# Kernel optimization log

Measured on AMD Instinct MI355X. Metric: run time of the kernel, lower is better.

Reference implementation:

```python
import jax, jax.numpy as jnp
import numpy as np

B, T, C, H = 2, 2048, 1024, 16
HD = C // H  # head_dim = 64


def setup_inputs() -> dict:
    key = jax.random.key(0)
    ks = jax.random.split(key, 5)
    x = jax.random.normal(ks[0], (B, T, C), dtype=jnp.float32)
    # realistic rotary tables: cos/sin of position*inv_freq, shape (T, HD//2)
    inv_freq = 1.0 / (10000.0 ** (jnp.arange(0, HD, 2, dtype=jnp.float32) / HD))
    ang = jnp.arange(T, dtype=jnp.float32)[:, None] * inv_freq[None, :]
    cos, sin = jnp.cos(ang), jnp.sin(ang)
    w_attn = jax.random.normal(ks[1], (C, 3 * C), dtype=jnp.float32) * (C ** -0.5)
    b_attn = jnp.zeros((3 * C,), dtype=jnp.float32)
    w_proj = jax.random.normal(ks[2], (C, C), dtype=jnp.float32) * (C ** -0.5)
    b_proj = jnp.zeros((C,), dtype=jnp.float32)
    return {"x": x, "cos": cos, "sin": sin, "w_attn": w_attn, "b_attn": b_attn,
            "w_proj": w_proj, "b_proj": b_proj}


def _apply_rotary(x, cos, sin):
    # x: (B, H, T, HD); cos/sin: (T, HD//2) broadcast over B,H
    x_even = x[..., ::2]
    x_odd = x[..., 1::2]
    rot = jnp.stack((x_even * cos - x_odd * sin, x_even * sin + x_odd * cos), axis=-1)
    return rot.reshape(*x.shape[:-1], x.shape[-1])


def reference(x, cos, sin, w_attn, b_attn, w_proj, b_proj):
    b, t, c = x.shape
    qkv = x @ w_attn + b_attn                       # (B, T, 3C)
    q, k, v = jnp.split(qkv, 3, axis=-1)
    # (B, T, C) -> (B, H, T, HD)
    def to_heads(z):
        return z.reshape(b, t, H, HD).transpose(0, 2, 1, 3)
    q, k, v = to_heads(q), to_heads(k), to_heads(v)
    q = _apply_rotary(q, cos, sin)
    k = _apply_rotary(k, cos, sin)
    scale = 1.0 / jnp.sqrt(jnp.asarray(HD, dtype=x.dtype))
    scores = jnp.einsum('bhqd,bhkd->bhqk', q, k) * scale
    causal = jnp.tril(jnp.ones((t, t), dtype=bool))
    scores = jnp.where(causal, scores, jnp.asarray(-jnp.inf, dtype=scores.dtype))
    attn = jax.nn.softmax(scores, axis=-1)
    y = jnp.einsum('bhqk,bhkd->bhqd', attn, v)      # (B, H, T, HD)
    y = y.transpose(0, 2, 1, 3).reshape(b, t, c)
    return y @ w_proj + b_proj
```

## Files before the change

kernel.cpp:

```cpp
#include <hip/hip_runtime.h>
#include <hip/hip_bf16.h>
#include <math.h>

#define Bsz 2
#define Tseq 2048
#define Cdim 1024
#define Hn 16
#define HDim 64
#define Mrows 4096
#define N3 3072
#define QSCALE 0.1803368801111137f

typedef __bf16 bf16_t;
typedef __bf16 bf16x4 __attribute__((ext_vector_type(4)));
typedef __bf16 bf16x8 __attribute__((ext_vector_type(8)));
typedef float floatx4 __attribute__((ext_vector_type(4)));

__device__ __forceinline__ void async16(const void* g, void* l) {
    __builtin_amdgcn_global_load_lds(
        (const __attribute__((address_space(1))) void*)g,
        (__attribute__((address_space(3))) void*)l, 16, 0, 0);
}

__global__ __launch_bounds__(256) void prep_kernel(
    const float* __restrict__ x, const float* __restrict__ w_attn,
    const float* __restrict__ w_proj, bf16_t* __restrict__ xb,
    bf16_t* __restrict__ waT, bf16_t* __restrict__ wpT)
{
    __shared__ float Ts[32][33];
    const int bid = blockIdx.x;
    if (bid < 2048) {
        size_t g = (size_t)bid * 256 + threadIdx.x;
        float4 a = *(const float4*)(x + g * 8);
        float4 b = *(const float4*)(x + g * 8 + 4);
        bf16x8 o;
        o[0] = (bf16_t)a.x; o[1] = (bf16_t)a.y; o[2] = (bf16_t)a.z; o[3] = (bf16_t)a.w;
        o[4] = (bf16_t)b.x; o[5] = (bf16_t)b.y; o[6] = (bf16_t)b.z; o[7] = (bf16_t)b.w;
        *(bf16x8*)(xb + g * 8) = o;
        return;
    }
    const float* in; bf16_t* out; int R, C, bx, by;
    if (bid < 5120) {
        int t = bid - 2048; in = w_attn; out = waT; R = Cdim; C = N3;
        bx = t % 96; by = t / 96;
    } else {
        int t = bid - 5120; in = w_proj; out = wpT; R = Cdim; C = Cdim;
        bx = t & 31; by = t >> 5;
    }
    int c0 = bx << 5, r0 = by << 5;
    int lr = threadIdx.x >> 3, lc = (threadIdx.x & 7) << 2;
    float4 v = *(const float4*)(in + (size_t)(r0 + lr) * C + c0 + lc);
    Ts[lr][lc] = v.x; Ts[lr][lc + 1] = v.y; Ts[lr][lc + 2] = v.z; Ts[lr][lc + 3] = v.w;
    __syncthreads();
    bf16x4 o;
    o[0] = (bf16_t)Ts[lc + 0][lr]; o[1] = (bf16_t)Ts[lc + 1][lr];
    o[2] = (bf16_t)Ts[lc + 2][lr]; o[3] = (bf16_t)Ts[lc + 3][lr];
    *(bf16x4*)(out + (size_t)(c0 + lr) * R + r0 + lc) = o;
}

__global__ __launch_bounds__(256) void gemm_qkv(
    const bf16_t* __restrict__ xb, const bf16_t* __restrict__ waT,
    const float* __restrict__ bias, const float* __restrict__ cosb,
    const float* __restrict__ sinb,
    bf16_t* __restrict__ qb, bf16_t* __restrict__ kb, bf16_t* __restrict__ vt)
{
    __shared__ bf16_t As[128 * 32];
    __shared__ bf16_t Bs[128 * 32];
    const int tid = threadIdx.x;
    const int lane = tid & 63, w = tid >> 6;
    const int lm = lane & 15, quad = lane >> 4;
    const int wy = w >> 1, wx = w & 1;
    const int m0 = blockIdx.y << 7, n0 = blockIdx.x << 7;

    const floatx4 fz = {0.f, 0.f, 0.f, 0.f};
    floatx4 acc[4][4];
    #pragma unroll
    for (int i = 0; i < 4; i++)
        #pragma unroll
        for (int j = 0; j < 4; j++) acc[i][j] = fz;

    const bf16_t* Ag = xb + (size_t)m0 * Cdim;
    const bf16_t* Bg = waT + (size_t)n0 * Cdim;

    for (int k0 = 0; k0 < Cdim; k0 += 32) {
        #pragma unroll
        for (int it = 0; it < 2; ++it) {
            int ci = (w << 7) + (it << 6) + lane;
            int row = ci >> 2, cq = (ci & 3) ^ (row & 3);
            async16(Ag + (size_t)row * Cdim + k0 + cq * 8, As + ((w << 7) + (it << 6)) * 8);
            async16(Bg + (size_t)row * Cdim + k0 + cq * 8, Bs + ((w << 7) + (it << 6)) * 8);
        }
        __syncthreads();
        bf16x8 af[4], bfr[4];
        #pragma unroll
        for (int i = 0; i < 4; i++) {
            int row = (wy << 6) + (i << 4) + lm;
            int cq = quad ^ (lm & 3);
            af[i] = *(const bf16x8*)&As[row * 32 + cq * 8];
        }
        #pragma unroll
        for (int j = 0; j < 4; j++) {
            int row = (wx << 6) + (j << 4) + lm;
            int cq = quad ^ (lm & 3);
            bfr[j] = *(const bf16x8*)&Bs[row * 32 + cq * 8];
        }
        #pragma unroll
        for (int i = 0; i < 4; i++)
            #pragma unroll
            for (int j = 0; j < 4; j++)
                acc[i][j] = __builtin_amdgcn_mfma_f32_16x16x32_bf16(af[i], bfr[j], acc[i][j], 0, 0, 0);
        __syncthreads();
    }

    const int sec = n0 >> 10;
    const int mb = m0 + (wy << 6);
    const int nb = n0 + (wx << 6);
    #pragma unroll
    for (int i = 0; i < 4; i++) {
        int mrow0 = mb + (i << 4) + (quad << 2);
        int b = mrow0 >> 11, t0 = mrow0 & 2047;
        #pragma unroll
        for (int j = 0; j < 4; j++) {
            int n = nb + (j << 4) + lm;
            float bi = bias[n];
            int rel = n & 1023;
            int h = rel >> 6, hd = rel & 63;
            if (sec == 2) {
                int tp = (t0 & ~31) | (((t0 >> 2) & 3) << 3) | (((t0 >> 4) & 1) << 2);
                bf16x4 pk;
                #pragma unroll
                for (int r = 0; r < 4; r++) pk[r] = (bf16_t)(acc[i][j][r] + bi);
                *(bf16x4*)&vt[((size_t)(b * Hn + h) * HDim + hd) * Tseq + tp] = pk;
            } else {
                bf16_t* dst = (sec == 0) ? qb : kb;
                const int ih = hd >> 1;
                const bool ev = !(hd & 1);
                #pragma unroll
                for (int r = 0; r < 4; r++) {
                    int t = t0 + r;
                    float v = acc[i][j][r] + bi;
                    float x = __shfl_xor(v, 1);
                    float c = cosb[t * 32 + ih], s = sinb[t * 32 + ih];
                    float rv = ev ? (v * c - x * s) : (x * s + v * c);
                    if (sec == 0) rv *= QSCALE;
                    dst[((size_t)(b * Hn + h) * Tseq + t) * HDim + hd] = (bf16_t)rv;
                }
            }
        }
    }
}

__global__ __launch_bounds__(256) void attn_mfma(
    const bf16_t* __restrict__ qb, const bf16_t* __restrict__ kb,
    const bf16_t* __restrict__ vt, bf16_t* __restrict__ yb)
{
    __shared__ bf16_t Ks[2][64 * 64];
    __shared__ bf16_t VTs[2][64 * 64];

    const int pp = blockIdx.x & 15;
    const int bh = blockIdx.x >> 4;
    const int b = bh >> 4, h = bh & 15;
    const int tid = threadIdx.x;
    const int w4 = tid >> 6, lane = tid & 63, lm = lane & 15, quad = lane >> 4;
    const int jt0 = pp, jt1 = 31 - pp;
    const int nk = 32 - pp;

    {
        const bf16_t* Kg = kb + (size_t)bh * Tseq * HDim;
        const bf16_t* Vg = vt + (size_t)bh * HDim * Tseq;
        #pragma unroll
        for (int it = 0; it < 2; ++it) {
            int ci = (it << 8) + tid;
            int row = ci >> 3, cq = (ci & 7) ^ (row & 7);
            async16(Kg + row * HDim + cq * 8, &Ks[0][((it << 8) + (w4 << 6)) * 8]);
            async16(Vg + (size_t)row * Tseq + cq * 8, &VTs[0][((it << 8) + (w4 << 6)) * 8]);
        }
    }

    bf16x8 qf[2][2];
    #pragma unroll
    for (int t = 0; t < 2; ++t) {
        int qrow = ((t ? jt1 : jt0) << 6) + (w4 << 4) + lm;
        const bf16_t* Qg = qb + ((size_t)bh * Tseq + qrow) * HDim;
        #pragma unroll
        for (int ks = 0; ks < 2; ++ks)
            qf[t][ks] = *(const bf16x8*)(Qg + (ks << 5) + (quad << 3));
    }
    __syncthreads();

    const floatx4 fz = {0.f, 0.f, 0.f, 0.f};
    floatx4 o_[2][4];
    #pragma unroll
    for (int t = 0; t < 2; ++t)
        #pragma unroll
        for (int f = 0; f < 4; ++f) o_[t][f] = fz;
    float l_[2] = {0.f, 0.f};
    const int lastk[2] = {pp, 31 - pp};
    const int qq[2] = {(jt0 << 6) + (w4 << 4) + lm, (jt1 << 6) + (w4 << 4) + lm};

    for (int kt = 0; kt < nk; ++kt) {
        const int cb = kt & 1;
        if (kt + 1 < nk) {
            const int nb2 = cb ^ 1;
            const bf16_t* Kg = kb + ((size_t)bh * Tseq + ((kt + 1) << 6)) * HDim;
            const bf16_t* Vg = vt + (size_t)bh * HDim * Tseq + ((kt + 1) << 6);
            #pragma unroll
            for (int it = 0; it < 2; ++it) {
                int ci = (it << 8) + tid;
                int row = ci >> 3, cq = (ci & 7) ^ (row & 7);
                async16(Kg + row * HDim + cq * 8, &Ks[nb2][((it << 8) + (w4 << 6)) * 8]);
                async16(Vg + (size_t)row * Tseq + cq * 8, &VTs[nb2][((it << 8) + (w4 << 6)) * 8]);
            }
        }

        floatx4 st[2][4];
        #pragma unroll
        for (int t = 0; t < 2; ++t)
            #pragma unroll
            for (int sub = 0; sub < 4; ++sub) st[t][sub] = fz;
        #pragma unroll
        for (int ks = 0; ks < 2; ++ks) {
            bf16x8 kf[4];
            #pragma unroll
            for (int sub = 0; sub < 4; ++sub) {
                int krow = (sub << 4) + lm;
                int kc = ((ks << 2) + quad) ^ (krow & 7);
                kf[sub] = *(const bf16x8*)&Ks[cb][krow * 64 + kc * 8];
            }
            if (kt <= lastk[0])
                #pragma unroll
                for (int sub = 0; sub < 4; ++sub)
                    st[0][sub] = __builtin_amdgcn_mfma_f32_16x16x32_bf16(
                        kf[sub], qf[0][ks], st[0][sub], 0, 0, 0);
            #pragma unroll
            for (int sub = 0; sub < 4; ++sub)
                st[1][sub] = __builtin_amdgcn_mfma_f32_16x16x32_bf16(
                    kf[sub], qf[1][ks], st[1][sub], 0, 0, 0);
        }

        bf16x8 pf[2][2];
        #pragma unroll
        for (int t = 0; t < 2; ++t) {
            if (kt > lastk[t]) continue;
            const bool dm = (kt == lastk[t]);
            float rs = 0.f;
            #pragma unroll
            for (int cc = 0; cc < 2; ++cc)
                #pragma unroll
                for (int jj = 0; jj < 8; ++jj) {
                    int sub = (cc << 1) + (jj >> 2), r = jj & 3;
                    float val = st[t][sub][r];
                    if (dm) {
                        int key = (kt << 6) + (sub << 4) + (quad << 2) + r;
                        if (key > qq[t]) val = -3e38f;
                    }
                    float p = exp2f(val);
                    rs += p;
                    pf[t][cc][jj] = (bf16_t)p;
                }
            rs += __shfl_xor(rs, 16);
            rs += __shfl_xor(rs, 32);
            l_[t] += rs;
        }

        #pragma unroll
        for (int cc = 0; cc < 2; ++cc) {
            bf16x8 vf[4];
            #pragma unroll
            for (int f = 0; f < 4; ++f) {
                int vrow = (f << 4) + lm;
                int vc = ((cc << 2) + quad) ^ (vrow & 7);
                vf[f] = *(const bf16x8*)&VTs[cb][vrow * 64 + vc * 8];
            }
            #pragma unroll
            for (int t = 0; t < 2; ++t) {
                if (kt > lastk[t]) continue;
                #pragma unroll
                for (int f = 0; f < 4; ++f)
                    o_[t][f] = __builtin_amdgcn_mfma_f32_16x16x32_bf16(
                        vf[f], pf[t][cc], o_[t][f], 0, 0, 0);
            }
        }
        __syncthreads();
    }

    #pragma unroll
    for (int t = 0; t < 2; ++t) {
        float inv = 1.f / l_[t];
        size_t base = ((size_t)(b * Tseq) + qq[t]) * Cdim + (h << 6) + (quad << 2);
        #pragma unroll
        for (int f = 0; f < 4; ++f) {
            bf16x4 ov;
            #pragma unroll
            for (int r = 0; r < 4; ++r) ov[r] = (bf16_t)(o_[t][f][r] * inv);
            *(bf16x4*)&yb[base + (f << 4)] = ov;
        }
    }
}

__global__ __launch_bounds__(256) void gemm_proj(
    const bf16_t* __restrict__ yb, const bf16_t* __restrict__ wpT,
    const float* __restrict__ bias, float* __restrict__ out)
{
    __shared__ bf16_t As[128 * 32];
    __shared__ bf16_t Bs[128 * 32];
    const int tid = threadIdx.x;
    const int lane = tid & 63, w = tid >> 6;
    const int lm = lane & 15, quad = lane >> 4;
    const int wy = w >> 1, wx = w & 1;
    const int m0 = blockIdx.y << 7, n0 = blockIdx.x << 7;

    const floatx4 fz = {0.f, 0.f, 0.f, 0.f};
    floatx4 acc[4][4];
    #pragma unroll
    for (int i = 0; i < 4; i++)
        #pragma unroll
        for (int j = 0; j < 4; j++) acc[i][j] = fz;

    const bf16_t* Ag = yb + (size_t)m0 * Cdim;
    const bf16_t* Bg = wpT + (size_t)n0 * Cdim;

    for (int k0 = 0; k0 < Cdim; k0 += 32) {
        #pragma unroll
        for (int it = 0; it < 2; ++it) {
            int ci = (w << 7) + (it << 6) + lane;
            int row = ci >> 2, cq = (ci & 3) ^ (row & 3);
            async16(Ag + (size_t)row * Cdim + k0 + cq * 8, As + ((w << 7) + (it << 6)) * 8);
            async16(Bg + (size_t)row * Cdim + k0 + cq * 8, Bs + ((w << 7) + (it << 6)) * 8);
        }
        __syncthreads();
        bf16x8 af[4], bfr[4];
        #pragma unroll
        for (int i = 0; i < 4; i++) {
            int row = (wy << 6) + (i << 4) + lm;
            int cq = quad ^ (lm & 3);
            af[i] = *(const bf16x8*)&As[row * 32 + cq * 8];
        }
        #pragma unroll
        for (int j = 0; j < 4; j++) {
            int row = (wx << 6) + (j << 4) + lm;
            int cq = quad ^ (lm & 3);
            bfr[j] = *(const bf16x8*)&Bs[row * 32 + cq * 8];
        }
        #pragma unroll
        for (int i = 0; i < 4; i++)
            #pragma unroll
            for (int j = 0; j < 4; j++)
                acc[i][j] = __builtin_amdgcn_mfma_f32_16x16x32_bf16(af[i], bfr[j], acc[i][j], 0, 0, 0);
        __syncthreads();
    }

    const int mb = m0 + (wy << 6);
    const int nb = n0 + (wx << 6);
    #pragma unroll
    for (int i = 0; i < 4; i++) {
        int mrow0 = mb + (i << 4) + (quad << 2);
        #pragma unroll
        for (int j = 0; j < 4; j++) {
            int n = nb + (j << 4) + lm;
            float bi = bias[n];
            #pragma unroll
            for (int r = 0; r < 4; r++)
                out[(size_t)(mrow0 + r) * Cdim + n] = acc[i][j][r] + bi;
        }
    }
}

extern "C" void kernel_launch(void* const* d_in, const int* in_sizes, int n_in,
                              void* d_out, int out_size, void* d_ws, size_t ws_size,
                              hipStream_t stream) {
    const float* x      = (const float*)d_in[0];
    const float* cosb   = (const float*)d_in[1];
    const float* sinb   = (const float*)d_in[2];
    const float* w_attn = (const float*)d_in[3];
    const float* b_attn = (const float*)d_in[4];
    const float* w_proj = (const float*)d_in[5];
    const float* b_proj = (const float*)d_in[6];

    char* ws = (char*)d_ws;
    bf16_t* xb  = (bf16_t*)(ws);
    bf16_t* waT = (bf16_t*)(ws + (size_t)(8 << 20));
    bf16_t* wpT = (bf16_t*)(ws + (size_t)(14 << 20));
    bf16_t* qb  = (bf16_t*)(ws + (size_t)(16 << 20));
    bf16_t* kb  = (bf16_t*)(ws + (size_t)(24 << 20));
    bf16_t* vtb = (bf16_t*)(ws + (size_t)(32 << 20));
    bf16_t* yb  = (bf16_t*)(ws + (size_t)(40 << 20));

    prep_kernel<<<6144, 256, 0, stream>>>(x, w_attn, w_proj, xb, waT, wpT);
    gemm_qkv<<<dim3(24, 32), 256, 0, stream>>>(xb, waT, b_attn, cosb, sinb, qb, kb, vtb);
    attn_mfma<<<512, 256, 0, stream>>>(qb, kb, vtb, yb);
    gemm_proj<<<dim3(8, 32), 256, 0, stream>>>(yb, wpT, b_proj, (float*)d_out);
}
```

Before: 205.6 us.

## Split paired causal query tiles into one block per tile, longest first

The attention kernel previously gave each block two query tiles (pp and 31-pp), sharing each K/V tile load between them to balance causal work. Now each block handles a single query tile, with 1024 blocks ordered so the longest tiles (largest jt) launch first. This lowers register pressure and raises parallelism, which may improve occupancy and tail balance. In exchange, blocks no longer share K/V loads across two query tiles, so LDS fill traffic per unit of compute roughly doubles.

```diff
diff --git a/kernel.cpp b/kernel.cpp
--- a/kernel.cpp
+++ b/kernel.cpp
@@ -157,13 +157,13 @@
     __shared__ bf16_t Ks[2][64 * 64];
     __shared__ bf16_t VTs[2][64 * 64];
 
-    const int pp = blockIdx.x & 15;
-    const int bh = blockIdx.x >> 4;
+    const int bid = blockIdx.x;
+    const int jt = 31 - (bid >> 5);
+    const int bh = bid & 31;
     const int b = bh >> 4, h = bh & 15;
     const int tid = threadIdx.x;
     const int w4 = tid >> 6, lane = tid & 63, lm = lane & 15, quad = lane >> 4;
-    const int jt0 = pp, jt1 = 31 - pp;
-    const int nk = 32 - pp;
+    const int nk = jt + 1;
 
     {
         const bf16_t* Kg = kb + (size_t)bh * Tseq * HDim;
@@ -177,26 +177,21 @@
         }
     }
 
-    bf16x8 qf[2][2];
-    #pragma unroll
-    for (int t = 0; t < 2; ++t) {
-        int qrow = ((t ? jt1 : jt0) << 6) + (w4 << 4) + lm;
-        const bf16_t* Qg = qb + ((size_t)bh * Tseq + qrow) * HDim;
+    const int qq = (jt << 6) + (w4 << 4) + lm;
+    bf16x8 qf[2];
+    {
+        const bf16_t* Qg = qb + ((size_t)bh * Tseq + qq) * HDim;
         #pragma unroll
         for (int ks = 0; ks < 2; ++ks)
-            qf[t][ks] = *(const bf16x8*)(Qg + (ks << 5) + (quad << 3));
+            qf[ks] = *(const bf16x8*)(Qg + (ks << 5) + (quad << 3));
     }
     __syncthreads();
 
     const floatx4 fz = {0.f, 0.f, 0.f, 0.f};
-    floatx4 o_[2][4];
-    #pragma unroll
-    for (int t = 0; t < 2; ++t)
-        #pragma unroll
-        for (int f = 0; f < 4; ++f) o_[t][f] = fz;
-    float l_[2] = {0.f, 0.f};
-    const int lastk[2] = {pp, 31 - pp};
-    const int qq[2] = {(jt0 << 6) + (w4 << 4) + lm, (jt1 << 6) + (w4 << 4) + lm};
+    floatx4 o_[4];
+    #pragma unroll
+    for (int f = 0; f < 4; ++f) o_[f] = fz;
+    float l_ = 0.f;
 
     for (int kt = 0; kt < nk; ++kt) {
         const int cb = kt & 1;
@@ -213,11 +208,9 @@
             }
         }
 
-        floatx4 st[2][4];
-        #pragma unroll
-        for (int t = 0; t < 2; ++t)
-            #pragma unroll
-            for (int sub = 0; sub < 4; ++sub) st[t][sub] = fz;
+        floatx4 st[4];
+        #pragma unroll
+        for (int sub = 0; sub < 4; ++sub) st[sub] = fz;
         #pragma unroll
         for (int ks = 0; ks < 2; ++ks) {
             bf16x8 kf[4];
@@ -227,41 +220,32 @@
                 int kc = ((ks << 2) + quad) ^ (krow & 7);
                 kf[sub] = *(const bf16x8*)&Ks[cb][krow * 64 + kc * 8];
             }
-            if (kt <= lastk[0])
-                #pragma unroll
-                for (int sub = 0; sub < 4; ++sub)
-                    st[0][sub] = __builtin_amdgcn_mfma_f32_16x16x32_bf16(
-                        kf[sub], qf[0][ks], st[0][sub], 0, 0, 0);
             #pragma unroll
             for (int sub = 0; sub < 4; ++sub)
-                st[1][sub] = __builtin_amdgcn_mfma_f32_16x16x32_bf16(
-                    kf[sub], qf[1][ks], st[1][sub], 0, 0, 0);
-        }
-
-        bf16x8 pf[2][2];
-        #pragma unroll
-        for (int t = 0; t < 2; ++t) {
-            if (kt > lastk[t]) continue;
-            const bool dm = (kt == lastk[t]);
-            float rs = 0.f;
-            #pragma unroll
-            for (int cc = 0; cc < 2; ++cc)
-                #pragma unroll
-                for (int jj = 0; jj < 8; ++jj) {
-                    int sub = (cc << 1) + (jj >> 2), r = jj & 3;
-                    float val = st[t][sub][r];
-                    if (dm) {
-                        int key = (kt << 6) + (sub << 4) + (quad << 2) + r;
-                        if (key > qq[t]) val = -3e38f;
-                    }
-                    float p = exp2f(val);
-                    rs += p;
-                    pf[t][cc][jj] = (bf16_t)p;
+                st[sub] = __builtin_amdgcn_mfma_f32_16x16x32_bf16(
+                    kf[sub], qf[ks], st[sub], 0, 0, 0);
+        }
+
+        const bool dm = (kt == jt);
+        bf16x8 pf[2];
+        float rs = 0.f;
+        #pragma unroll
+        for (int cc = 0; cc < 2; ++cc)
+            #pragma unroll
+            for (int jj = 0; jj < 8; ++jj) {
+                int sub = (cc << 1) + (jj >> 2), r = jj & 3;
+                float val = st[sub][r];
+                if (dm) {
+                    int key = (kt << 6) + (sub << 4) + (quad << 2) + r;
+                    if (key > qq) val = -3e38f;
                 }
-            rs += __shfl_xor(rs, 16);
-            rs += __shfl_xor(rs, 32);
-            l_[t] += rs;
-        }
+                float p = exp2f(val);
+                rs += p;
+                pf[cc][jj] = (bf16_t)p;
+            }
+        rs += __shfl_xor(rs, 16);
+        rs += __shfl_xor(rs, 32);
+        l_ += rs;
 
         #pragma unroll
         for (int cc = 0; cc < 2; ++cc) {
@@ -273,26 +257,21 @@
                 vf[f] = *(const bf16x8*)&VTs[cb][vrow * 64 + vc * 8];
             }
             #pragma unroll
-            for (int t = 0; t < 2; ++t) {
-                if (kt > lastk[t]) continue;
-                #pragma unroll
-                for (int f = 0; f < 4; ++f)
-                    o_[t][f] = __builtin_amdgcn_mfma_f32_16x16x32_bf16(
-                        vf[f], pf[t][cc], o_[t][f], 0, 0, 0);
-            }
-        }
-        __syncthreads();
-    }
-
-    #pragma unroll
-    for (int t = 0; t < 2; ++t) {
-        float inv = 1.f / l_[t];
-        size_t base = ((size_t)(b * Tseq) + qq[t]) * Cdim + (h << 6) + (quad << 2);
+            for (int f = 0; f < 4; ++f)
+                o_[f] = __builtin_amdgcn_mfma_f32_16x16x32_bf16(
+                    vf[f], pf[cc], o_[f], 0, 0, 0);
+        }
+        __syncthreads();
+    }
+
+    {
+        float inv = 1.f / l_;
+        size_t base = ((size_t)(b * Tseq) + qq) * Cdim + (h << 6) + (quad << 2);
         #pragma unroll
         for (int f = 0; f < 4; ++f) {
             bf16x4 ov;
             #pragma unroll
-            for (int r = 0; r < 4; ++r) ov[r] = (bf16_t)(o_[t][f][r] * inv);
+            for (int r = 0; r < 4; ++r) ov[r] = (bf16_t)(o_[f][r] * inv);
             *(bf16x4*)&yb[base + (f << 4)] = ov;
         }
     }
@@ -388,6 +367,6 @@
 
     prep_kernel<<<6144, 256, 0, stream>>>(x, w_attn, w_proj, xb, waT, wpT);
     gemm_qkv<<<dim3(24, 32), 256, 0, stream>>>(xb, waT, b_attn, cosb, sinb, qb, kb, vtb);
-    attn_mfma<<<512, 256, 0, stream>>>(qb, kb, vtb, yb);
+    attn_mfma<<<1024, 256, 0, stream>>>(qb, kb, vtb, yb);
     gemm_proj<<<dim3(8, 32), 256, 0, stream>>>(yb, wpT, b_proj, (float*)d_out);
 }
```

Result: faster. 186.1 us (-9.5%).
